# Kernel tuning notes

Measured on AMD Instinct MI355X. Metric: run time of the kernel, lower is better.

The kernel has to match this reference:

```python
import jax, jax.numpy as jnp
import numpy as np

N = 100_000   # nodes
E = 1_600_000 # edges
IN, H, OUT = 128, 128, 128
G = 64        # graphs in batch
EPS = 1e-5    # batchnorm eps


def setup_inputs() -> dict:
    key = jax.random.key(0)
    ks = jax.random.split(key, 16)
    x = jax.random.normal(ks[0], (N, IN), dtype=jnp.float32)
    edge_index = jax.random.randint(ks[1], (2, E), 0, N, dtype=jnp.int32)
    batch = jnp.sort(jax.random.randint(ks[2], (N,), 0, G, dtype=jnp.int32))
    def lin(k, fi, fo):
        return jax.random.normal(k, (fi, fo), dtype=jnp.float32) / np.sqrt(fi).astype(np.float32)
    inp = {
        'x': x, 'edge_index': edge_index, 'batch': batch,
        'W1': lin(ks[3], IN, H), 'b1': jnp.zeros((H,), jnp.float32),
        'g1': jnp.ones((H,), jnp.float32), 'beta1': jnp.zeros((H,), jnp.float32),
        'W2': lin(ks[4], H, H), 'b2': jnp.zeros((H,), jnp.float32),
        'g2': jnp.ones((H,), jnp.float32), 'beta2': jnp.zeros((H,), jnp.float32),
        'W3': lin(ks[5], H, H), 'b3': jnp.zeros((H,), jnp.float32),
        'g3': jnp.ones((H,), jnp.float32), 'beta3': jnp.zeros((H,), jnp.float32),
        'fc_w': lin(ks[6], H, OUT), 'fc_b': jnp.zeros((OUT,), jnp.float32),
    }
    return inp


def _gcn_prep(edge_index):
    # add self loops, compute symmetric normalization (shared across layers)
    loop = jnp.arange(N, dtype=edge_index.dtype)
    row = jnp.concatenate([edge_index[0], loop])  # source
    col = jnp.concatenate([edge_index[1], loop])  # target
    deg = jax.ops.segment_sum(jnp.ones_like(col, dtype=jnp.float32), col, num_segments=N)
    dinv = jnp.where(deg > 0, jax.lax.rsqrt(deg), 0.0)
    norm = dinv[row] * dinv[col]  # (E+N,)
    return row, col, norm


def _gcn_bn_relu(h, W, b, g, beta, row, col, norm):
    hw = h @ W                                           # (N, H)
    msg = norm[:, None] * hw[row]                        # gather + scale
    h = jax.ops.segment_sum(msg, col, num_segments=N) + b  # scatter-add
    # BatchNorm1d (training-mode batch statistics, biased var)
    mu = jnp.mean(h, axis=0)
    var = jnp.mean(jnp.square(h - mu), axis=0)
    h = g * (h - mu) * jax.lax.rsqrt(var + EPS) + beta
    return jax.nn.relu(h)


def reference(x, edge_index, batch, W1, b1, g1, beta1, W2, b2, g2, beta2,
              W3, b3, g3, beta3, fc_w, fc_b):
    row, col, norm = _gcn_prep(edge_index)
    h = _gcn_bn_relu(x, W1, b1, g1, beta1, row, col, norm)
    h = _gcn_bn_relu(h, W2, b2, g2, beta2, row, col, norm)
    h = _gcn_bn_relu(h, W3, b3, g3, beta3, row, col, norm)
    # global_mean_pool over batch assignment
    sums = jax.ops.segment_sum(h, batch, num_segments=G)
    cnt = jax.ops.segment_sum(jnp.ones((N,), jnp.float32), batch, num_segments=G)
    pooled = sums / jnp.maximum(cnt, 1.0)[:, None]       # (G, H)
    return pooled @ fc_w + fc_b                          # (G, OUT)
```

## Files before the change

### kernel.cpp

```cpp
#include <hip/hip_runtime.h>

#define NN 100000
#define EE 1600000
#define HH 128
#define GG 64
#define TOT (EE + NN)
#define PSPLIT 8
#define NB 782
#define BCAP 4096
#define FCHUNK 4096

typedef __attribute__((ext_vector_type(8))) short s16x8;
typedef __attribute__((ext_vector_type(4))) float f32x4;

__device__ __forceinline__ unsigned short f2bf(float f) {
    unsigned u = __float_as_uint(f);
    u = u + 0x7FFFu + ((u >> 16) & 1u);
    return (unsigned short)(u >> 16);
}


__global__ __launch_bounds__(256) void setup_kernel(const float* __restrict__ x,
                                                    const int* __restrict__ batch,
                                                    const float* __restrict__ W0,
                                                    const float* __restrict__ W1,
                                                    const float* __restrict__ W2,
                                                    unsigned* __restrict__ Xbf,
                                                    int* __restrict__ cursor,
                                                    int* __restrict__ gstart, int* __restrict__ gend,
                                                    float* __restrict__ poolsum,
                                                    unsigned short* __restrict__ Wt) {
    int i = blockIdx.x * 256 + threadIdx.x;
    if (i < NN * 64) {
        float2 v = ((const float2*)x)[i];
        Xbf[i] = (unsigned)f2bf(v.x) | ((unsigned)f2bf(v.y) << 16);
    }
    if (i < NB) cursor[i] = i * BCAP;
    if (i < GG * HH) poolsum[i] = 0.f;
    if (i < GG) {
        int lo = 0, hi = NN;
        while (lo < hi) { int m = (lo + hi) >> 1; if (batch[m] < i) lo = m + 1; else hi = m; }
        int s = lo;
        lo = 0; hi = NN;
        while (lo < hi) { int m = (lo + hi) >> 1; if (batch[m] < i + 1) lo = m + 1; else hi = m; }
        gstart[i] = s;
        gend[i] = lo;
    }
    if (i < 3 * HH * HH) {
        int l = i >> 14, r = i & 16383;
        const float* W = (l == 0) ? W0 : (l == 1) ? W1 : W2;
        int k = r >> 7, n = r & 127;
        Wt[l * HH * HH + n * HH + k] = f2bf(W[r]);
    }
}

__global__ __launch_bounds__(256) void bfill2_kernel(const int* __restrict__ ei, int* cursor,
                                                     unsigned* __restrict__ ebuf) {
    __shared__ int h[NB];
    __shared__ int lbase[NB];
    int tid = threadIdx.x;
    size_t e0 = (size_t)blockIdx.x * FCHUNK;
    for (int i = tid; i < NB; i += 256) h[i] = 0;
    __syncthreads();
    unsigned r[16], c[16];
#pragma unroll
    for (int k = 0; k < 16; ++k) {
        size_t e = e0 + (size_t)k * 256 + tid;
        unsigned rr = 0xFFFFFFFFu, cc = 0;
        if (e < EE) {
            rr = (unsigned)ei[e];
            cc = (unsigned)ei[EE + e];
            if (rr >= NN || cc >= NN) rr = 0xFFFFFFFFu;
        }
        r[k] = rr; c[k] = cc;
        if (rr != 0xFFFFFFFFu) atomicAdd(&h[cc >> 7], 1);
    }
    __syncthreads();
    for (int i = tid; i < NB; i += 256) {
        int cnt = h[i];
        lbase[i] = cnt ? atomicAdd(&cursor[i], cnt) : 0;
    }
    __syncthreads();
    for (int i = tid; i < NB; i += 256) h[i] = 0;
    __syncthreads();
#pragma unroll
    for (int k = 0; k < 16; ++k) {
        if (r[k] != 0xFFFFFFFFu) {
            unsigned cc = c[k];
            int b = cc >> 7;
            int slot = lbase[b] + atomicAdd(&h[b], 1);
            if (slot >= b * BCAP && slot < (b + 1) * BCAP)
                ebuf[slot] = (r[k] << 7) | (cc & 127u);
        }
    }
}

__global__ void bscan_kernel(const int* __restrict__ cursor, int* __restrict__ bucketSlotStart,
                             int* __restrict__ col_start) {
    __shared__ int ss[1024];
    int t = threadIdx.x;
    int ec = 0, nc = 0;
    if (t < NB) {
        ec = min(max(cursor[t] - t * BCAP, 0), BCAP);
        nc = min(128, NN - t * 128);
    }
    ss[t] = ec + nc;
    __syncthreads();
    for (int off = 1; off < 1024; off <<= 1) {
        int a = 0;
        if (t >= off) a = ss[t - off];
        __syncthreads();
        ss[t] += a;
        __syncthreads();
    }
    if (t < NB) bucketSlotStart[t] = ss[t] - (ec + nc);
    if (t == NB - 1) col_start[NN] = ss[t];
}

__global__ __launch_bounds__(256) void bproc_kernel(const unsigned* __restrict__ ebuf,
                                                    const int* __restrict__ cursor,
                                                    const int* __restrict__ bucketSlotStart,
                                                    int* __restrict__ col_start,
                                                    float* __restrict__ dinv,
                                                    int* __restrict__ srcv) {
    __shared__ unsigned s_e[BCAP];
    __shared__ int s_cnt[128], s_scan[128], s_cur[128];
    int b = blockIdx.x;
    int tid = threadIdx.x;
    int n0 = b * 128;
    int nb = min(128, NN - n0);
    int est = b * BCAP;
    int ecnt = min(max(cursor[b] - est, 0), BCAP);
    if (tid < 128) s_cnt[tid] = 0;
    __syncthreads();
    for (int i = tid; i < ecnt; i += 256) {
        unsigned v = ebuf[est + i];
        s_e[i] = v;
        atomicAdd(&s_cnt[v & 127u], 1);
    }
    __syncthreads();
    int myc = 0;
    if (tid < 128) {
        myc = (tid < nb) ? s_cnt[tid] + 1 : 0;
        s_scan[tid] = myc;
    }
    __syncthreads();
    for (int off = 1; off < 128; off <<= 1) {
        int a = 0;
        if (tid < 128 && tid >= off) a = s_scan[tid - off];
        __syncthreads();
        if (tid < 128) s_scan[tid] += a;
        __syncthreads();
    }
    if (tid < nb) {
        int slotbase = bucketSlotStart[b] + s_scan[tid] - myc;
        col_start[n0 + tid] = slotbase;
        dinv[n0 + tid] = rsqrtf((float)(s_cnt[tid] + 1));
        srcv[slotbase] = n0 + tid;
        s_cur[tid] = slotbase + 1;
    }
    __syncthreads();
    for (int i = tid; i < ecnt; i += 256) {
        unsigned v = s_e[i];
        int slot = atomicAdd(&s_cur[v & 127u], 1);
        srcv[slot] = (int)(v >> 7);
    }
}


__global__ __launch_bounds__(256) void agg_kernel(const uint4* __restrict__ Xbf4,
                                                  const int* __restrict__ col_start,
                                                  const int* __restrict__ srcv,
                                                  const float* __restrict__ dinv,
                                                  unsigned short* __restrict__ Abf,
                                                  float* __restrict__ gsum,
                                                  float* __restrict__ gsq) {
    if (blockIdx.x == 0 && threadIdx.x < HH) {
        gsum[threadIdx.x] = 0.f;
        gsq[threadIdx.x] = 0.f;
    }
    int wv = (int)((blockIdx.x * blockDim.x + threadIdx.x) >> 6);
    int lane = threadIdx.x & 63;
    int half = lane >> 5;
    int node = 2 * wv + half;
    if (2 * wv >= NN) return;
    bool valid = node < NN;
    int s0 = 0, s1 = 0;
    float dd = 0.f;
    if (valid) { s0 = col_start[node]; s1 = col_start[node + 1]; dd = dinv[node]; }
    int lane31 = lane & 31;
    int qh = (lane >> 4) & 1;
    int l16 = lane & 15;
    float acc[8];
#pragma unroll
    for (int j = 0; j < 8; ++j) acc[j] = 0.f;

    for (int base = s0; base < s1; base += 32) {
        int cnt = min(32, s1 - base);
        int msrc = 0;
        float mw = 0.f;
        if (lane31 < cnt) { msrc = srcv[base + lane31]; mw = dinv[msrc] * dd; }
        int rounds = (cnt + 1) >> 1;
        int rp = ((rounds + 5) / 6) * 6;
        for (int p = 0; p < rp; p += 6) {
            uint4 u[6];
            float w[6];
#pragma unroll
            for (int k = 0; k < 6; ++k) {
                int idx = (p + k) * 2 + qh;
                int sl = half * 32 + min(idx, 31);
                int src = __shfl(msrc, sl);
                float wk = __shfl(mw, sl);
                if (idx > 31) wk = 0.f;
                w[k] = wk;
                u[k] = Xbf4[(size_t)src * 16 + l16];
            }
#pragma unroll
            for (int k = 0; k < 6; ++k) {
                acc[0] += w[k] * __uint_as_float(u[k].x << 16);
                acc[1] += w[k] * __uint_as_float(u[k].x & 0xFFFF0000u);
                acc[2] += w[k] * __uint_as_float(u[k].y << 16);
                acc[3] += w[k] * __uint_as_float(u[k].y & 0xFFFF0000u);
                acc[4] += w[k] * __uint_as_float(u[k].z << 16);
                acc[5] += w[k] * __uint_as_float(u[k].z & 0xFFFF0000u);
                acc[6] += w[k] * __uint_as_float(u[k].w << 16);
                acc[7] += w[k] * __uint_as_float(u[k].w & 0xFFFF0000u);
            }
        }
    }
#pragma unroll
    for (int j = 0; j < 8; ++j) acc[j] += __shfl_xor(acc[j], 16);
    if ((lane & 16) == 0 && valid) {
        uint4 pk;
        pk.x = (unsigned)f2bf(acc[0]) | ((unsigned)f2bf(acc[1]) << 16);
        pk.y = (unsigned)f2bf(acc[2]) | ((unsigned)f2bf(acc[3]) << 16);
        pk.z = (unsigned)f2bf(acc[4]) | ((unsigned)f2bf(acc[5]) << 16);
        pk.w = (unsigned)f2bf(acc[6]) | ((unsigned)f2bf(acc[7]) << 16);
        ((uint4*)Abf)[(size_t)node * 16 + l16] = pk;
    }
}

__global__ __launch_bounds__(256) void gemm_stats_kernel(const unsigned short* __restrict__ Abf,
                                                         const unsigned short* __restrict__ Wt,
                                                         const float* __restrict__ bias,
                                                         float* __restrict__ gsum,
                                                         float* __restrict__ gsq) {
    __shared__ unsigned short wlds[128 * 136];
    __shared__ float ssum[HH], ssq[HH];
    int tid = threadIdx.x;
    if (tid < HH) { ssum[tid] = 0.f; ssq[tid] = 0.f; }
#pragma unroll
    for (int it = 0; it < 16; ++it) {
        int idx = it * 256 + tid;
        int r = idx >> 5, c = idx & 31;
        *(uint2*)&wlds[r * 136 + c * 4] = *(const uint2*)(Wt + r * HH + c * 4);
    }
    __syncthreads();

    int lane = tid & 63;
    int wave = tid >> 6;
    int mcol = lane & 15;
    int quad = lane >> 4;
    int rowbase = blockIdx.x * 128 + wave * 32;
    int row0 = rowbase + mcol;
    int row1 = row0 + 16;

    f32x4 acc[2][8];
#pragma unroll
    for (int mt = 0; mt < 2; ++mt)
#pragma unroll
        for (int nt = 0; nt < 8; ++nt) acc[mt][nt] = (f32x4){0.f, 0.f, 0.f, 0.f};

    s16x8 zf = {0, 0, 0, 0, 0, 0, 0, 0};
#pragma unroll
    for (int ks = 0; ks < 4; ++ks) {
        int k0 = ks * 32 + quad * 8;
        s16x8 a0 = (row0 < NN) ? *(const s16x8*)(Abf + (size_t)row0 * HH + k0) : zf;
        s16x8 a1 = (row1 < NN) ? *(const s16x8*)(Abf + (size_t)row1 * HH + k0) : zf;
#pragma unroll
        for (int nt = 0; nt < 8; ++nt) {
            s16x8 b = *(const s16x8*)&wlds[(nt * 16 + mcol) * 136 + k0];
            acc[0][nt] = __builtin_amdgcn_mfma_f32_16x16x32_bf16(a0, b, acc[0][nt], 0, 0, 0);
            acc[1][nt] = __builtin_amdgcn_mfma_f32_16x16x32_bf16(a1, b, acc[1][nt], 0, 0, 0);
        }
    }

    float s[8], sq[8];
#pragma unroll
    for (int nt = 0; nt < 8; ++nt) { s[nt] = 0.f; sq[nt] = 0.f; }
#pragma unroll
    for (int mt = 0; mt < 2; ++mt) {
        int rbase = rowbase + mt * 16 + quad * 4;
#pragma unroll
        for (int nt = 0; nt < 8; ++nt) {
            float bv = bias[nt * 16 + mcol];
            f32x4 a = acc[mt][nt];
#pragma unroll
            for (int reg = 0; reg < 4; ++reg) {
                if (rbase + reg < NN) {
                    float h = a[reg] + bv;
                    s[nt] += h; sq[nt] += h * h;
                }
            }
        }
    }
#pragma unroll
    for (int nt = 0; nt < 8; ++nt) {
        float v = s[nt];  v += __shfl_xor(v, 16);  v += __shfl_xor(v, 32);
        float w = sq[nt]; w += __shfl_xor(w, 16);  w += __shfl_xor(w, 32);
        if (quad == 0) {
            atomicAdd(&ssum[nt * 16 + mcol], v);
            atomicAdd(&ssq[nt * 16 + mcol], w);
        }
    }
    __syncthreads();
    if (tid < HH) {
        atomicAdd(&gsum[tid], ssum[tid]);
        atomicAdd(&gsq[tid], ssq[tid]);
    }
}

__global__ __launch_bounds__(256) void gemm_apply_kernel(const unsigned short* __restrict__ Abf,
                                                         const unsigned short* __restrict__ Wt,
                                                         const float* __restrict__ bias,
                                                         const float* __restrict__ gsum,
                                                         const float* __restrict__ gsq,
                                                         const float* __restrict__ g,
                                                         const float* __restrict__ beta,
                                                         unsigned short* __restrict__ Xb16) {
    __shared__ unsigned short wlds[128 * 136];
    __shared__ float asc[HH], bsh[HH];
    int tid = threadIdx.x;
#pragma unroll
    for (int it = 0; it < 16; ++it) {
        int idx = it * 256 + tid;
        int r = idx >> 5, c = idx & 31;
        *(uint2*)&wlds[r * 136 + c * 4] = *(const uint2*)(Wt + r * HH + c * 4);
    }
    if (tid < HH) {
        float mu = gsum[tid] * (1.f / (float)NN);
        float var = fmaxf(gsq[tid] * (1.f / (float)NN) - mu * mu, 0.f);
        float a = g[tid] * rsqrtf(var + 1e-5f);
        asc[tid] = a;
        bsh[tid] = a * (bias[tid] - mu) + beta[tid];
    }
    __syncthreads();

    int lane = tid & 63;
    int wave = tid >> 6;
    int mcol = lane & 15;
    int quad = lane >> 4;
    int rowbase = blockIdx.x * 128 + wave * 32;
    int row0 = rowbase + mcol;
    int row1 = row0 + 16;

    f32x4 acc[2][8];
#pragma unroll
    for (int mt = 0; mt < 2; ++mt)
#pragma unroll
        for (int nt = 0; nt < 8; ++nt) acc[mt][nt] = (f32x4){0.f, 0.f, 0.f, 0.f};

    s16x8 zf = {0, 0, 0, 0, 0, 0, 0, 0};
#pragma unroll
    for (int ks = 0; ks < 4; ++ks) {
        int k0 = ks * 32 + quad * 8;
        s16x8 a0 = (row0 < NN) ? *(const s16x8*)(Abf + (size_t)row0 * HH + k0) : zf;
        s16x8 a1 = (row1 < NN) ? *(const s16x8*)(Abf + (size_t)row1 * HH + k0) : zf;
#pragma unroll
        for (int nt = 0; nt < 8; ++nt) {
            s16x8 b = *(const s16x8*)&wlds[(nt * 16 + mcol) * 136 + k0];
            acc[0][nt] = __builtin_amdgcn_mfma_f32_16x16x32_bf16(a0, b, acc[0][nt], 0, 0, 0);
            acc[1][nt] = __builtin_amdgcn_mfma_f32_16x16x32_bf16(a1, b, acc[1][nt], 0, 0, 0);
        }
    }

#pragma unroll
    for (int mt = 0; mt < 2; ++mt) {
        int rbase = rowbase + mt * 16 + quad * 4;
#pragma unroll
        for (int nt = 0; nt < 8; ++nt) {
            int col = nt * 16 + mcol;
            float av = asc[col], bv = bsh[col];
            f32x4 a = acc[mt][nt];
#pragma unroll
            for (int reg = 0; reg < 4; ++reg) {
                int r = rbase + reg;
                if (r < NN) {
                    float o = fmaxf(av * a[reg] + bv, 0.f);
                    Xb16[(size_t)r * HH + col] = f2bf(o);
                }
            }
        }
    }
}


__global__ void pool_kernel(const unsigned* __restrict__ Xbf, const int* __restrict__ gstart,
                            const int* __restrict__ gend, float* __restrict__ poolsum) {
    int g = blockIdx.x;
    int sp = blockIdx.y;
    int t = threadIdx.x;
    int s = gstart[g], e = gend[g];
    if (e <= s) return;
    int len = e - s;
    int chunk = (len + PSPLIT - 1) / PSPLIT;
    int cs = s + sp * chunk;
    int ce = min(cs + chunk, e);
    if (cs >= ce) return;
    float2 acc = make_float2(0.f, 0.f);
    for (int i = cs; i < ce; ++i) {
        unsigned u = Xbf[(size_t)i * 64 + t];
        acc.x += __uint_as_float(u << 16);
        acc.y += __uint_as_float(u & 0xFFFF0000u);
    }
    atomicAdd(&poolsum[g * HH + 2 * t], acc.x);
    atomicAdd(&poolsum[g * HH + 2 * t + 1], acc.y);
}

__global__ void fc_kernel(const float* __restrict__ poolsum, const int* __restrict__ gstart,
                          const int* __restrict__ gend, const float* __restrict__ fc_w,
                          const float* __restrict__ fc_b, float* __restrict__ out) {
    int g = blockIdx.x;
    int o = threadIdx.x;
    int cnt = gend[g] - gstart[g];
    float inv = (cnt > 0) ? (1.f / (float)cnt) : 0.f;
    float acc = fc_b[o];
    for (int k = 0; k < HH; ++k) acc += (poolsum[g * HH + k] * inv) * fc_w[k * HH + o];
    out[g * HH + o] = acc;
}


extern "C" void kernel_launch(void* const* d_in, const int* in_sizes, int n_in,
                              void* d_out, int out_size, void* d_ws, size_t ws_size,
                              hipStream_t stream) {
    const float* x     = (const float*)d_in[0];
    const int*   ei    = (const int*)d_in[1];
    const int*   batch = (const int*)d_in[2];
    const float* Wl[3]    = {(const float*)d_in[3], (const float*)d_in[7], (const float*)d_in[11]};
    const float* bl[3]    = {(const float*)d_in[4], (const float*)d_in[8], (const float*)d_in[12]};
    const float* gl[3]    = {(const float*)d_in[5], (const float*)d_in[9], (const float*)d_in[13]};
    const float* betal[3] = {(const float*)d_in[6], (const float*)d_in[10], (const float*)d_in[14]};
    const float* fc_w = (const float*)d_in[15];
    const float* fc_b = (const float*)d_in[16];
    float* out = (float*)d_out;

    char* ws = (char*)d_ws;
    size_t off = 0;
    auto take = [&](size_t n) -> void* {
        void* p = ws + off;
        off = (off + n + 255) & ~(size_t)255;
        return p;
    };
    int*   bucketSlotStart = (int*)take((size_t)NB * 4);
    int*   cursor          = (int*)take((size_t)NB * 4);
    unsigned* ebuf         = (unsigned*)take((size_t)NB * BCAP * 4);
    int*   col_start       = (int*)take((size_t)(NN + 1) * 4);
    float* dinv            = (float*)take((size_t)NN * 4);
    int*   srcv            = (int*)take((size_t)TOT * 4);
    float* gsum            = (float*)take(HH * 4);
    float* gsq             = (float*)take(HH * 4);
    int*   gstart          = (int*)take(GG * 4);
    int*   gend            = (int*)take(GG * 4);
    float* poolsum         = (float*)take((size_t)GG * HH * 4);
    unsigned short* wt     = (unsigned short*)take((size_t)3 * HH * HH * 2);
    unsigned* Xbf          = (unsigned*)take((size_t)NN * 64 * 4);
    unsigned short* Abf    = (unsigned short*)take((size_t)NN * HH * 2);

    setup_kernel<<<(NN * 64 + 255) / 256, 256, 0, stream>>>(x, batch, Wl[0], Wl[1], Wl[2],
                                                            Xbf, cursor, gstart, gend, poolsum, wt);
    bfill2_kernel<<<(EE + FCHUNK - 1) / FCHUNK, 256, 0, stream>>>(ei, cursor, ebuf);
    bscan_kernel<<<1, 1024, 0, stream>>>(cursor, bucketSlotStart, col_start);
    bproc_kernel<<<NB, 256, 0, stream>>>(ebuf, cursor, bucketSlotStart, col_start, dinv, srcv);

    const int aggBlocks = (((NN + 1) / 2) * 64 + 255) / 256;
    for (int l = 0; l < 3; ++l) {
        const unsigned short* W = wt + (size_t)l * HH * HH;
        agg_kernel<<<aggBlocks, 256, 0, stream>>>((const uint4*)Xbf, col_start, srcv,
                                                  dinv, Abf, gsum, gsq);
        gemm_stats_kernel<<<(NN + 127) / 128, 256, 0, stream>>>(Abf, W, bl[l], gsum, gsq);
        gemm_apply_kernel<<<(NN + 127) / 128, 256, 0, stream>>>(Abf, W, bl[l], gsum, gsq,
                                                                gl[l], betal[l],
                                                                (unsigned short*)Xbf);
    }

    pool_kernel<<<dim3(GG, PSPLIT), 64, 0, stream>>>(Xbf, gstart, gend, poolsum);
    fc_kernel<<<GG, 128, 0, stream>>>(poolsum, gstart, gend, fc_w, fc_b, out);
}
```

Baseline: 549.4 us.

## Fuse GEMM stats and BN-apply into one cooperative kernel with grid sync

Replaces the separate stats and apply GEMM passes with one cooperative kernel. It computes the MFMA GEMM once, accumulates batchnorm sums globally, grid-syncs, then applies normalization and ReLU from registers. This avoids recomputing the GEMM and re-reading Abf and the weights in a second launch. It depends on all 782 blocks being co-resident (launch bounds 256,4) and falls back to the two-kernel path if the cooperative launch fails. The store pattern writes single bf16 values rather than packed vectors.

Result: slower. 766.3 us (+39.5%).

```diff
diff --git a/kernel.cpp b/kernel.cpp
--- a/kernel.cpp
+++ b/kernel.cpp
@@ -1,4 +1,7 @@
 #include <hip/hip_runtime.h>
+#include <hip/hip_cooperative_groups.h>
+
+namespace cg = cooperative_groups;
 
 #define NN 100000
 #define EE 1600000
@@ -239,6 +242,124 @@
         ((uint4*)Abf)[(size_t)node * 16 + l16] = pk;
     }
 }
+
+__global__ __launch_bounds__(256, 4) void gemm_fused_kernel(const unsigned short* __restrict__ Abf,
+                                                            const unsigned short* __restrict__ Wt,
+                                                            const float* __restrict__ bias,
+                                                            float* __restrict__ gsum,
+                                                            float* __restrict__ gsq,
+                                                            const float* __restrict__ g,
+                                                            const float* __restrict__ beta,
+                                                            unsigned short* __restrict__ Xb16) {
+    __shared__ unsigned short wlds[128 * 136];
+    __shared__ float ssum[HH], ssq[HH];
+    __shared__ float asc[HH], bsh[HH];
+    int tid = threadIdx.x;
+    if (tid < HH) { ssum[tid] = 0.f; ssq[tid] = 0.f; }
+#pragma unroll
+    for (int it = 0; it < 16; ++it) {
+        int idx = it * 256 + tid;
+        int r = idx >> 5, c = idx & 31;
+        *(uint2*)&wlds[r * 136 + c * 4] = *(const uint2*)(Wt + r * HH + c * 4);
+    }
+    __syncthreads();
+
+    int lane = tid & 63;
+    int wave = tid >> 6;
+    int mcol = lane & 15;
+    int quad = lane >> 4;
+    int rowbase = blockIdx.x * 128 + wave * 32;
+    int row0 = rowbase + mcol;
+    int row1 = row0 + 16;
+
+    f32x4 acc[2][8];
+#pragma unroll
+    for (int mt = 0; mt < 2; ++mt)
+#pragma unroll
+        for (int nt = 0; nt < 8; ++nt) acc[mt][nt] = (f32x4){0.f, 0.f, 0.f, 0.f};
+
+    s16x8 zf = {0, 0, 0, 0, 0, 0, 0, 0};
+#pragma unroll
+    for (int ks = 0; ks < 4; ++ks) {
+        int k0 = ks * 32 + quad * 8;
+        s16x8 a0 = (row0 < NN) ? *(const s16x8*)(Abf + (size_t)row0 * HH + k0) : zf;
+        s16x8 a1 = (row1 < NN) ? *(const s16x8*)(Abf + (size_t)row1 * HH + k0) : zf;
+#pragma unroll
+        for (int nt = 0; nt < 8; ++nt) {
+            s16x8 b = *(const s16x8*)&wlds[(nt * 16 + mcol) * 136 + k0];
+            acc[0][nt] = __builtin_amdgcn_mfma_f32_16x16x32_bf16(a0, b, acc[0][nt], 0, 0, 0);
+            acc[1][nt] = __builtin_amdgcn_mfma_f32_16x16x32_bf16(a1, b, acc[1][nt], 0, 0, 0);
+        }
+    }
+
+    float s[8], sq[8];
+#pragma unroll
+    for (int nt = 0; nt < 8; ++nt) { s[nt] = 0.f; sq[nt] = 0.f; }
+#pragma unroll
+    for (int mt = 0; mt < 2; ++mt) {
+        int rbase = rowbase + mt * 16 + quad * 4;
+#pragma unroll
+        for (int nt = 0; nt < 8; ++nt) {
+            float bv = bias[nt * 16 + mcol];
+            f32x4 a = acc[mt][nt];
+#pragma unroll
+            for (int reg = 0; reg < 4; ++reg) {
+                if (rbase + reg < NN) {
+                    float h = a[reg] + bv;
+                    s[nt] += h; sq[nt] += h * h;
+                }
+            }
+        }
+    }
+#pragma unroll
+    for (int nt = 0; nt < 8; ++nt) {
+        float v = s[nt];  v += __shfl_xor(v, 16);  v += __shfl_xor(v, 32);
+        float w = sq[nt]; w += __shfl_xor(w, 16);  w += __shfl_xor(w, 32);
+        if (quad == 0) {
+            atomicAdd(&ssum[nt * 16 + mcol], v);
+            atomicAdd(&ssq[nt * 16 + mcol], w);
+        }
+    }
+    __syncthreads();
+    if (tid < HH) {
+        atomicAdd(&gsum[tid], ssum[tid]);
+        atomicAdd(&gsq[tid], ssq[tid]);
+    }
+    __threadfence();
+
+    cg::this_grid().sync();
+
+    if (tid < HH) {
+        float gs = __hip_atomic_load(&gsum[tid], __ATOMIC_RELAXED, __HIP_MEMORY_SCOPE_AGENT);
+        float gq = __hip_atomic_load(&gsq[tid], __ATOMIC_RELAXED, __HIP_MEMORY_SCOPE_AGENT);
+        float mu = gs * (1.f / (float)NN);
+        float var = fmaxf(gq * (1.f / (float)NN) - mu * mu, 0.f);
+        float a = g[tid] * rsqrtf(var + 1e-5f);
+        asc[tid] = a;
+        bsh[tid] = a * (bias[tid] - mu) + beta[tid];
+    }
+    __syncthreads();
+
+#pragma unroll
+    for (int mt = 0; mt < 2; ++mt) {
+        int rbase = rowbase + mt * 16 + quad * 4;
+#pragma unroll
+        for (int nt = 0; nt < 8; ++nt) {
+            int col = nt * 16 + mcol;
+            float av = asc[col], bv = bsh[col];
+            f32x4 a = acc[mt][nt];
+#pragma unroll
+            for (int reg = 0; reg < 4; ++reg) {
+                int r = rbase + reg;
+                if (r < NN) {
+                    float o = fmaxf(av * a[reg] + bv, 0.f);
+                    Xb16[(size_t)r * HH + col] = f2bf(o);
+                }
+            }
+        }
+    }
+}
+
 
 __global__ __launch_bounds__(256) void gemm_stats_kernel(const unsigned short* __restrict__ Abf,
                                                          const unsigned short* __restrict__ Wt,
@@ -475,12 +596,23 @@
     const int aggBlocks = (((NN + 1) / 2) * 64 + 255) / 256;
     for (int l = 0; l < 3; ++l) {
         const unsigned short* W = wt + (size_t)l * HH * HH;
+        const float* bias = bl[l];
+        const float* gg = gl[l];
+        const float* bb = betal[l];
+        unsigned short* xout = (unsigned short*)Xbf;
         agg_kernel<<<aggBlocks, 256, 0, stream>>>((const uint4*)Xbf, col_start, srcv,
                                                   dinv, Abf, gsum, gsq);
-        gemm_stats_kernel<<<(NN + 127) / 128, 256, 0, stream>>>(Abf, W, bl[l], gsum, gsq);
-        gemm_apply_kernel<<<(NN + 127) / 128, 256, 0, stream>>>(Abf, W, bl[l], gsum, gsq,
-                                                                gl[l], betal[l],
-                                                                (unsigned short*)Xbf);
+        void* args[] = {(void*)&Abf, (void*)&W, (void*)&bias, (void*)&gsum, (void*)&gsq,
+                        (void*)&gg, (void*)&bb, (void*)&xout};
+        hipError_t cerr = hipLaunchCooperativeKernel((void*)gemm_fused_kernel,
+                                                     dim3((NN + 127) / 128), dim3(256),
+                                                     args, 0, stream);
+        if (cerr != hipSuccess) {
+            (void)hipGetLastError();
+            gemm_stats_kernel<<<(NN + 127) / 128, 256, 0, stream>>>(Abf, W, bias, gsum, gsq);
+            gemm_apply_kernel<<<(NN + 127) / 128, 256, 0, stream>>>(Abf, W, bias, gsum, gsq,
+                                                                    gg, bb, xout);
+        }
     }
 
     pool_kernel<<<dim3(GG, PSPLIT), 64, 0, stream>>>(Xbf, gstart, gend, poolsum);
```

## Store GEMM output in stats pass and replace recompute with elementwise BN-ReLU

Applied to the files above, without the earlier changes.

The stats GEMM now writes its bf16 result back in place over the aggregated input, and a new grid-stride elementwise kernel applies batchnorm scale/shift and ReLU, removing the second GEMM pass and its weight staging. The weight tile in LDS is also reordered into MFMA fragment order for contiguous 16-byte reads. This trades a recomputed matmul for an extra bf16 write and read of the hidden activations, adds an extra rounding before normalization, and uses narrow 2-byte scattered stores.

New measurement: 576.8 us. 5.0% more time.

```diff
diff --git a/kernel.cpp b/kernel.cpp
--- a/kernel.cpp
+++ b/kernel.cpp
@@ -240,20 +240,22 @@
     }
 }
 
-__global__ __launch_bounds__(256) void gemm_stats_kernel(const unsigned short* __restrict__ Abf,
+__global__ __launch_bounds__(256) void gemm_stats_kernel(unsigned short* __restrict__ Abf,
                                                          const unsigned short* __restrict__ Wt,
                                                          const float* __restrict__ bias,
                                                          float* __restrict__ gsum,
                                                          float* __restrict__ gsq) {
-    __shared__ unsigned short wlds[128 * 136];
+    __shared__ unsigned short wlds[2048 * 8];
     __shared__ float ssum[HH], ssq[HH];
     int tid = threadIdx.x;
     if (tid < HH) { ssum[tid] = 0.f; ssq[tid] = 0.f; }
 #pragma unroll
-    for (int it = 0; it < 16; ++it) {
-        int idx = it * 256 + tid;
-        int r = idx >> 5, c = idx & 31;
-        *(uint2*)&wlds[r * 136 + c * 4] = *(const uint2*)(Wt + r * HH + c * 4);
+    for (int it = 0; it < 8; ++it) {
+        int c = it * 256 + tid;
+        int n = c & 127, k8 = c >> 7;
+        int nt = n >> 4, mcol = n & 15, ks = k8 >> 2, quad = k8 & 3;
+        int dst = (nt * 16 + ks * 4 + quad) * 16 + mcol;
+        *(uint4*)&wlds[dst * 8] = *(const uint4*)(Wt + n * HH + k8 * 8);
     }
     __syncthreads();
 
@@ -279,12 +281,14 @@
         s16x8 a1 = (row1 < NN) ? *(const s16x8*)(Abf + (size_t)row1 * HH + k0) : zf;
 #pragma unroll
         for (int nt = 0; nt < 8; ++nt) {
-            s16x8 b = *(const s16x8*)&wlds[(nt * 16 + mcol) * 136 + k0];
+            s16x8 b = *(const s16x8*)&wlds[((nt * 16 + ks * 4 + quad) * 16 + mcol) * 8];
             acc[0][nt] = __builtin_amdgcn_mfma_f32_16x16x32_bf16(a0, b, acc[0][nt], 0, 0, 0);
             acc[1][nt] = __builtin_amdgcn_mfma_f32_16x16x32_bf16(a1, b, acc[1][nt], 0, 0, 0);
         }
     }
 
+    __syncthreads();
+
     float s[8], sq[8];
 #pragma unroll
     for (int nt = 0; nt < 8; ++nt) { s[nt] = 0.f; sq[nt] = 0.f; }
@@ -293,13 +297,16 @@
         int rbase = rowbase + mt * 16 + quad * 4;
 #pragma unroll
         for (int nt = 0; nt < 8; ++nt) {
-            float bv = bias[nt * 16 + mcol];
+            int col = nt * 16 + mcol;
+            float bv = bias[col];
             f32x4 a = acc[mt][nt];
 #pragma unroll
             for (int reg = 0; reg < 4; ++reg) {
-                if (rbase + reg < NN) {
+                int r = rbase + reg;
+                if (r < NN) {
                     float h = a[reg] + bv;
                     s[nt] += h; sq[nt] += h * h;
+                    Abf[(size_t)r * HH + col] = f2bf(a[reg]);
                 }
             }
         }
@@ -320,23 +327,15 @@
     }
 }
 
-__global__ __launch_bounds__(256) void gemm_apply_kernel(const unsigned short* __restrict__ Abf,
-                                                         const unsigned short* __restrict__ Wt,
-                                                         const float* __restrict__ bias,
-                                                         const float* __restrict__ gsum,
-                                                         const float* __restrict__ gsq,
-                                                         const float* __restrict__ g,
-                                                         const float* __restrict__ beta,
-                                                         unsigned short* __restrict__ Xb16) {
-    __shared__ unsigned short wlds[128 * 136];
+__global__ __launch_bounds__(256) void bnrelu_kernel(const uint4* __restrict__ Hb,
+                                                     const float* __restrict__ bias,
+                                                     const float* __restrict__ gsum,
+                                                     const float* __restrict__ gsq,
+                                                     const float* __restrict__ g,
+                                                     const float* __restrict__ beta,
+                                                     uint4* __restrict__ Xbf) {
     __shared__ float asc[HH], bsh[HH];
     int tid = threadIdx.x;
-#pragma unroll
-    for (int it = 0; it < 16; ++it) {
-        int idx = it * 256 + tid;
-        int r = idx >> 5, c = idx & 31;
-        *(uint2*)&wlds[r * 136 + c * 4] = *(const uint2*)(Wt + r * HH + c * 4);
-    }
     if (tid < HH) {
         float mu = gsum[tid] * (1.f / (float)NN);
         float var = fmaxf(gsq[tid] * (1.f / (float)NN) - mu * mu, 0.f);
@@ -345,52 +344,29 @@
         bsh[tid] = a * (bias[tid] - mu) + beta[tid];
     }
     __syncthreads();
-
-    int lane = tid & 63;
-    int wave = tid >> 6;
-    int mcol = lane & 15;
-    int quad = lane >> 4;
-    int rowbase = blockIdx.x * 128 + wave * 32;
-    int row0 = rowbase + mcol;
-    int row1 = row0 + 16;
-
-    f32x4 acc[2][8];
-#pragma unroll
-    for (int mt = 0; mt < 2; ++mt)
-#pragma unroll
-        for (int nt = 0; nt < 8; ++nt) acc[mt][nt] = (f32x4){0.f, 0.f, 0.f, 0.f};
-
-    s16x8 zf = {0, 0, 0, 0, 0, 0, 0, 0};
-#pragma unroll
-    for (int ks = 0; ks < 4; ++ks) {
-        int k0 = ks * 32 + quad * 8;
-        s16x8 a0 = (row0 < NN) ? *(const s16x8*)(Abf + (size_t)row0 * HH + k0) : zf;
-        s16x8 a1 = (row1 < NN) ? *(const s16x8*)(Abf + (size_t)row1 * HH + k0) : zf;
-#pragma unroll
-        for (int nt = 0; nt < 8; ++nt) {
-            s16x8 b = *(const s16x8*)&wlds[(nt * 16 + mcol) * 136 + k0];
-            acc[0][nt] = __builtin_amdgcn_mfma_f32_16x16x32_bf16(a0, b, acc[0][nt], 0, 0, 0);
-            acc[1][nt] = __builtin_amdgcn_mfma_f32_16x16x32_bf16(a1, b, acc[1][nt], 0, 0, 0);
-        }
-    }
-
-#pragma unroll
-    for (int mt = 0; mt < 2; ++mt) {
-        int rbase = rowbase + mt * 16 + quad * 4;
-#pragma unroll
-        for (int nt = 0; nt < 8; ++nt) {
-            int col = nt * 16 + mcol;
-            float av = asc[col], bv = bsh[col];
-            f32x4 a = acc[mt][nt];
-#pragma unroll
-            for (int reg = 0; reg < 4; ++reg) {
-                int r = rbase + reg;
-                if (r < NN) {
-                    float o = fmaxf(av * a[reg] + bv, 0.f);
-                    Xb16[(size_t)r * HH + col] = f2bf(o);
-                }
-            }
-        }
+    int stride = gridDim.x * 256;
+    for (int e = blockIdx.x * 256 + tid; e < NN * 16; e += stride) {
+        uint4 u = Hb[e];
+        int c0 = (e & 15) * 8;
+        uint4 o;
+        float h0, h1, o0, o1;
+        h0 = __uint_as_float(u.x << 16);  h1 = __uint_as_float(u.x & 0xFFFF0000u);
+        o0 = fmaxf(fmaf(asc[c0 + 0], h0, bsh[c0 + 0]), 0.f);
+        o1 = fmaxf(fmaf(asc[c0 + 1], h1, bsh[c0 + 1]), 0.f);
+        o.x = (unsigned)f2bf(o0) | ((unsigned)f2bf(o1) << 16);
+        h0 = __uint_as_float(u.y << 16);  h1 = __uint_as_float(u.y & 0xFFFF0000u);
+        o0 = fmaxf(fmaf(asc[c0 + 2], h0, bsh[c0 + 2]), 0.f);
+        o1 = fmaxf(fmaf(asc[c0 + 3], h1, bsh[c0 + 3]), 0.f);
+        o.y = (unsigned)f2bf(o0) | ((unsigned)f2bf(o1) << 16);
+        h0 = __uint_as_float(u.z << 16);  h1 = __uint_as_float(u.z & 0xFFFF0000u);
+        o0 = fmaxf(fmaf(asc[c0 + 4], h0, bsh[c0 + 4]), 0.f);
+        o1 = fmaxf(fmaf(asc[c0 + 5], h1, bsh[c0 + 5]), 0.f);
+        o.z = (unsigned)f2bf(o0) | ((unsigned)f2bf(o1) << 16);
+        h0 = __uint_as_float(u.w << 16);  h1 = __uint_as_float(u.w & 0xFFFF0000u);
+        o0 = fmaxf(fmaf(asc[c0 + 6], h0, bsh[c0 + 6]), 0.f);
+        o1 = fmaxf(fmaf(asc[c0 + 7], h1, bsh[c0 + 7]), 0.f);
+        o.w = (unsigned)f2bf(o0) | ((unsigned)f2bf(o1) << 16);
+        Xbf[e] = o;
     }
 }
 
@@ -478,9 +454,8 @@
         agg_kernel<<<aggBlocks, 256, 0, stream>>>((const uint4*)Xbf, col_start, srcv,
                                                   dinv, Abf, gsum, gsq);
         gemm_stats_kernel<<<(NN + 127) / 128, 256, 0, stream>>>(Abf, W, bl[l], gsum, gsq);
-        gemm_apply_kernel<<<(NN + 127) / 128, 256, 0, stream>>>(Abf, W, bl[l], gsum, gsq,
-                                                                gl[l], betal[l],
-                                                                (unsigned short*)Xbf);
+        bnrelu_kernel<<<2048, 256, 0, stream>>>((const uint4*)Abf, bl[l], gsum, gsq,
+                                                gl[l], betal[l], (uint4*)Xbf);
     }
 
     pool_kernel<<<dim3(GG, PSPLIT), 64, 0, stream>>>(Xbf, gstart, gend, poolsum);
```

## Process two row tiles per GEMM block with prefetched A and fragment-ordered W

Applied to the files above, without the earlier changes.

Both GEMM kernels now cover 256 rows per block in two 128-row sub-tiles, so each block stages the weight matrix into LDS once for twice as many rows. The A fragments for the second sub-tile are loaded while the first sub-tile's MFMAs and epilogue run. W is stored in LDS in MFMA-fragment order so each lane's B reads are contiguous, and occupancy is hinted at three blocks per CU. The cost is more registers for the double-buffered A fragments and half as many blocks in the grid.

After: 560.0 us. About the same (+1.9%).

```diff
diff --git a/kernel.cpp b/kernel.cpp
--- a/kernel.cpp
+++ b/kernel.cpp
@@ -9,6 +9,7 @@
 #define NB 782
 #define BCAP 4096
 #define FCHUNK 4096
+#define GBLK ((NN + 255) / 256)
 
 typedef __attribute__((ext_vector_type(8))) short s16x8;
 typedef __attribute__((ext_vector_type(4))) float f32x4;
@@ -240,70 +241,96 @@
     }
 }
 
-__global__ __launch_bounds__(256) void gemm_stats_kernel(const unsigned short* __restrict__ Abf,
-                                                         const unsigned short* __restrict__ Wt,
-                                                         const float* __restrict__ bias,
-                                                         float* __restrict__ gsum,
-                                                         float* __restrict__ gsq) {
-    __shared__ unsigned short wlds[128 * 136];
+__device__ __forceinline__ void stage_w_frag(unsigned short* wlds,
+                                             const unsigned short* __restrict__ Wt, int tid) {
+#pragma unroll
+    for (int it = 0; it < 8; ++it) {
+        int c = it * 256 + tid;
+        int n = c & 127, k8 = c >> 7;
+        int nt = n >> 4, mcol = n & 15, ks = k8 >> 2, quad = k8 & 3;
+        int dst = (nt * 16 + ks * 4 + quad) * 16 + mcol;
+        *(uint4*)&wlds[dst * 8] = *(const uint4*)(Wt + n * HH + k8 * 8);
+    }
+}
+
+__device__ __forceinline__ void load_a(const unsigned short* __restrict__ Abf,
+                                       int row0, int row1, s16x8* a0, s16x8* a1, int quad) {
+    s16x8 zf = {0, 0, 0, 0, 0, 0, 0, 0};
+#pragma unroll
+    for (int ks = 0; ks < 4; ++ks) {
+        int k0 = ks * 32 + quad * 8;
+        a0[ks] = (row0 < NN) ? *(const s16x8*)(Abf + (size_t)row0 * HH + k0) : zf;
+        a1[ks] = (row1 < NN) ? *(const s16x8*)(Abf + (size_t)row1 * HH + k0) : zf;
+    }
+}
+
+__global__ __launch_bounds__(256, 3) void gemm_stats_kernel(const unsigned short* __restrict__ Abf,
+                                                            const unsigned short* __restrict__ Wt,
+                                                            const float* __restrict__ bias,
+                                                            float* __restrict__ gsum,
+                                                            float* __restrict__ gsq) {
+    __shared__ unsigned short wlds[2048 * 8];
     __shared__ float ssum[HH], ssq[HH];
     int tid = threadIdx.x;
     if (tid < HH) { ssum[tid] = 0.f; ssq[tid] = 0.f; }
-#pragma unroll
-    for (int it = 0; it < 16; ++it) {
-        int idx = it * 256 + tid;
-        int r = idx >> 5, c = idx & 31;
-        *(uint2*)&wlds[r * 136 + c * 4] = *(const uint2*)(Wt + r * HH + c * 4);
-    }
-    __syncthreads();
+    stage_w_frag(wlds, Wt, tid);
 
     int lane = tid & 63;
     int wave = tid >> 6;
     int mcol = lane & 15;
     int quad = lane >> 4;
-    int rowbase = blockIdx.x * 128 + wave * 32;
-    int row0 = rowbase + mcol;
-    int row1 = row0 + 16;
-
-    f32x4 acc[2][8];
-#pragma unroll
-    for (int mt = 0; mt < 2; ++mt)
-#pragma unroll
-        for (int nt = 0; nt < 8; ++nt) acc[mt][nt] = (f32x4){0.f, 0.f, 0.f, 0.f};
-
-    s16x8 zf = {0, 0, 0, 0, 0, 0, 0, 0};
-#pragma unroll
-    for (int ks = 0; ks < 4; ++ks) {
-        int k0 = ks * 32 + quad * 8;
-        s16x8 a0 = (row0 < NN) ? *(const s16x8*)(Abf + (size_t)row0 * HH + k0) : zf;
-        s16x8 a1 = (row1 < NN) ? *(const s16x8*)(Abf + (size_t)row1 * HH + k0) : zf;
-#pragma unroll
-        for (int nt = 0; nt < 8; ++nt) {
-            s16x8 b = *(const s16x8*)&wlds[(nt * 16 + mcol) * 136 + k0];
-            acc[0][nt] = __builtin_amdgcn_mfma_f32_16x16x32_bf16(a0, b, acc[0][nt], 0, 0, 0);
-            acc[1][nt] = __builtin_amdgcn_mfma_f32_16x16x32_bf16(a1, b, acc[1][nt], 0, 0, 0);
-        }
-    }
+    int rowbase0 = blockIdx.x * 256 + wave * 32;
+
+    s16x8 a0c[4], a1c[4], a0n[4], a1n[4];
+    load_a(Abf, rowbase0 + mcol, rowbase0 + mcol + 16, a0c, a1c, quad);
+    __syncthreads();
 
     float s[8], sq[8];
 #pragma unroll
     for (int nt = 0; nt < 8; ++nt) { s[nt] = 0.f; sq[nt] = 0.f; }
-#pragma unroll
-    for (int mt = 0; mt < 2; ++mt) {
-        int rbase = rowbase + mt * 16 + quad * 4;
-#pragma unroll
-        for (int nt = 0; nt < 8; ++nt) {
-            float bv = bias[nt * 16 + mcol];
-            f32x4 a = acc[mt][nt];
-#pragma unroll
-            for (int reg = 0; reg < 4; ++reg) {
-                if (rbase + reg < NN) {
-                    float h = a[reg] + bv;
-                    s[nt] += h; sq[nt] += h * h;
+
+#pragma unroll
+    for (int sub = 0; sub < 2; ++sub) {
+        int rowbase = rowbase0 + sub * 128;
+        f32x4 acc[2][8];
+#pragma unroll
+        for (int mt = 0; mt < 2; ++mt)
+#pragma unroll
+            for (int nt = 0; nt < 8; ++nt) acc[mt][nt] = (f32x4){0.f, 0.f, 0.f, 0.f};
+#pragma unroll
+        for (int ks = 0; ks < 4; ++ks) {
+#pragma unroll
+            for (int nt = 0; nt < 8; ++nt) {
+                s16x8 b = *(const s16x8*)&wlds[((nt * 16 + ks * 4 + quad) * 16 + mcol) * 8];
+                acc[0][nt] = __builtin_amdgcn_mfma_f32_16x16x32_bf16(a0c[ks], b, acc[0][nt], 0, 0, 0);
+                acc[1][nt] = __builtin_amdgcn_mfma_f32_16x16x32_bf16(a1c[ks], b, acc[1][nt], 0, 0, 0);
+            }
+        }
+        if (sub == 0) {
+            load_a(Abf, rowbase0 + 128 + mcol, rowbase0 + 128 + mcol + 16, a0n, a1n, quad);
+        }
+#pragma unroll
+        for (int mt = 0; mt < 2; ++mt) {
+            int rbase = rowbase + mt * 16 + quad * 4;
+#pragma unroll
+            for (int nt = 0; nt < 8; ++nt) {
+                float bv = bias[nt * 16 + mcol];
+                f32x4 a = acc[mt][nt];
+#pragma unroll
+                for (int reg = 0; reg < 4; ++reg) {
+                    if (rbase + reg < NN) {
+                        float h = a[reg] + bv;
+                        s[nt] += h; sq[nt] += h * h;
+                    }
                 }
             }
         }
-    }
+        if (sub == 0) {
+#pragma unroll
+            for (int ks = 0; ks < 4; ++ks) { a0c[ks] = a0n[ks]; a1c[ks] = a1n[ks]; }
+        }
+    }
+
 #pragma unroll
     for (int nt = 0; nt < 8; ++nt) {
         float v = s[nt];  v += __shfl_xor(v, 16);  v += __shfl_xor(v, 32);
@@ -320,23 +347,18 @@
     }
 }
 
-__global__ __launch_bounds__(256) void gemm_apply_kernel(const unsigned short* __restrict__ Abf,
-                                                         const unsigned short* __restrict__ Wt,
-                                                         const float* __restrict__ bias,
-                                                         const float* __restrict__ gsum,
-                                                         const float* __restrict__ gsq,
-                                                         const float* __restrict__ g,
-                                                         const float* __restrict__ beta,
-                                                         unsigned short* __restrict__ Xb16) {
-    __shared__ unsigned short wlds[128 * 136];
+__global__ __launch_bounds__(256, 3) void gemm_apply_kernel(const unsigned short* __restrict__ Abf,
+                                                            const unsigned short* __restrict__ Wt,
+                                                            const float* __restrict__ bias,
+                                                            const float* __restrict__ gsum,
+                                                            const float* __restrict__ gsq,
+                                                            const float* __restrict__ g,
+                                                            const float* __restrict__ beta,
+                                                            unsigned short* __restrict__ Xb16) {
+    __shared__ unsigned short wlds[2048 * 8];
     __shared__ float asc[HH], bsh[HH];
     int tid = threadIdx.x;
-#pragma unroll
-    for (int it = 0; it < 16; ++it) {
-        int idx = it * 256 + tid;
-        int r = idx >> 5, c = idx & 31;
-        *(uint2*)&wlds[r * 136 + c * 4] = *(const uint2*)(Wt + r * HH + c * 4);
-    }
+    stage_w_frag(wlds, Wt, tid);
     if (tid < HH) {
         float mu = gsum[tid] * (1.f / (float)NN);
         float var = fmaxf(gsq[tid] * (1.f / (float)NN) - mu * mu, 0.f);
@@ -344,52 +366,58 @@
         asc[tid] = a;
         bsh[tid] = a * (bias[tid] - mu) + beta[tid];
     }
-    __syncthreads();
 
     int lane = tid & 63;
     int wave = tid >> 6;
     int mcol = lane & 15;
     int quad = lane >> 4;
-    int rowbase = blockIdx.x * 128 + wave * 32;
-    int row0 = rowbase + mcol;
-    int row1 = row0 + 16;
-
-    f32x4 acc[2][8];
-#pragma unroll
-    for (int mt = 0; mt < 2; ++mt)
-#pragma unroll
-        for (int nt = 0; nt < 8; ++nt) acc[mt][nt] = (f32x4){0.f, 0.f, 0.f, 0.f};
-
-    s16x8 zf = {0, 0, 0, 0, 0, 0, 0, 0};
-#pragma unroll
-    for (int ks = 0; ks < 4; ++ks) {
-        int k0 = ks * 32 + quad * 8;
-        s16x8 a0 = (row0 < NN) ? *(const s16x8*)(Abf + (size_t)row0 * HH + k0) : zf;
-        s16x8 a1 = (row1 < NN) ? *(const s16x8*)(Abf + (size_t)row1 * HH + k0) : zf;
-#pragma unroll
-        for (int nt = 0; nt < 8; ++nt) {
-            s16x8 b = *(const s16x8*)&wlds[(nt * 16 + mcol) * 136 + k0];
-            acc[0][nt] = __builtin_amdgcn_mfma_f32_16x16x32_bf16(a0, b, acc[0][nt], 0, 0, 0);
-            acc[1][nt] = __builtin_amdgcn_mfma_f32_16x16x32_bf16(a1, b, acc[1][nt], 0, 0, 0);
-        }
-    }
-
-#pragma unroll
-    for (int mt = 0; mt < 2; ++mt) {
-        int rbase = rowbase + mt * 16 + quad * 4;
-#pragma unroll
-        for (int nt = 0; nt < 8; ++nt) {
-            int col = nt * 16 + mcol;
-            float av = asc[col], bv = bsh[col];
-            f32x4 a = acc[mt][nt];
-#pragma unroll
-            for (int reg = 0; reg < 4; ++reg) {
-                int r = rbase + reg;
-                if (r < NN) {
-                    float o = fmaxf(av * a[reg] + bv, 0.f);
-                    Xb16[(size_t)r * HH + col] = f2bf(o);
+    int rowbase0 = blockIdx.x * 256 + wave * 32;
+
+    s16x8 a0c[4], a1c[4], a0n[4], a1n[4];
+    load_a(Abf, rowbase0 + mcol, rowbase0 + mcol + 16, a0c, a1c, quad);
+    __syncthreads();
+
+#pragma unroll
+    for (int sub = 0; sub < 2; ++sub) {
+        int rowbase = rowbase0 + sub * 128;
+        f32x4 acc[2][8];
+#pragma unroll
+        for (int mt = 0; mt < 2; ++mt)
+#pragma unroll
+            for (int nt = 0; nt < 8; ++nt) acc[mt][nt] = (f32x4){0.f, 0.f, 0.f, 0.f};
+#pragma unroll
+        for (int ks = 0; ks < 4; ++ks) {
+#pragma unroll
+            for (int nt = 0; nt < 8; ++nt) {
+                s16x8 b = *(const s16x8*)&wlds[((nt * 16 + ks * 4 + quad) * 16 + mcol) * 8];
+                acc[0][nt] = __builtin_amdgcn_mfma_f32_16x16x32_bf16(a0c[ks], b, acc[0][nt], 0, 0, 0);
+                acc[1][nt] = __builtin_amdgcn_mfma_f32_16x16x32_bf16(a1c[ks], b, acc[1][nt], 0, 0, 0);
+            }
+        }
+        if (sub == 0) {
+            load_a(Abf, rowbase0 + 128 + mcol, rowbase0 + 128 + mcol + 16, a0n, a1n, quad);
+        }
+#pragma unroll
+        for (int mt = 0; mt < 2; ++mt) {
+            int rbase = rowbase + mt * 16 + quad * 4;
+#pragma unroll
+            for (int nt = 0; nt < 8; ++nt) {
+                int col = nt * 16 + mcol;
+                float av = asc[col], bv = bsh[col];
+                f32x4 a = acc[mt][nt];
+#pragma unroll
+                for (int reg = 0; reg < 4; ++reg) {
+                    int r = rbase + reg;
+                    if (r < NN) {
+                        float o = fmaxf(av * a[reg] + bv, 0.f);
+                        Xb16[(size_t)r * HH + col] = f2bf(o);
+                    }
                 }
             }
+        }
+        if (sub == 0) {
+#pragma unroll
+            for (int ks = 0; ks < 4; ++ks) { a0c[ks] = a0n[ks]; a1c[ks] = a1n[ks]; }
         }
     }
 }
@@ -477,10 +505,9 @@
         const unsigned short* W = wt + (size_t)l * HH * HH;
         agg_kernel<<<aggBlocks, 256, 0, stream>>>((const uint4*)Xbf, col_start, srcv,
                                                   dinv, Abf, gsum, gsq);
-        gemm_stats_kernel<<<(NN + 127) / 128, 256, 0, stream>>>(Abf, W, bl[l], gsum, gsq);
-        gemm_apply_kernel<<<(NN + 127) / 128, 256, 0, stream>>>(Abf, W, bl[l], gsum, gsq,
-                                                                gl[l], betal[l],
-                                                                (unsigned short*)Xbf);
+        gemm_stats_kernel<<<GBLK, 256, 0, stream>>>(Abf, W, bl[l], gsum, gsq);
+        gemm_apply_kernel<<<GBLK, 256, 0, stream>>>(Abf, W, bl[l], gsum, gsq,
+                                                    gl[l], betal[l], (unsigned short*)Xbf);
     }
 
     pool_kernel<<<dim3(GG, PSPLIT), 64, 0, stream>>>(Xbf, gstart, gend, poolsum);
```
